# Optimization experiments

Measured on AMD Instinct MI355X. Metric: run time of the kernel, lower is better.

The kernel has to match this reference:

```python
import jax, jax.numpy as jnp
import numpy as np

B, S, I, H = 64, 1024, 256, 256  # batch, seq_len, input_size, hidden_size (2 layers)


def _gru_layer(x, W_ih, W_hh, b_ih, b_hh):
    """Run a torch.nn.GRUCell-equivalent layer over time. x: [B,S,in] -> [B,S,H]."""
    Hd = W_hh.shape[1]
    # Precompute input-side gate projections for all timesteps (math-equivalent).
    xg = jnp.einsum('bsi,gi->bsg', x, W_ih) + b_ih  # [B,S,3H]

    def step(h, xg_t):
        hg = h @ W_hh.T + b_hh                      # [B,3H]
        xr, xz, xn = jnp.split(xg_t, 3, axis=-1)
        hr, hz, hn = jnp.split(hg, 3, axis=-1)
        r = jax.nn.sigmoid(xr + hr)
        z = jax.nn.sigmoid(xz + hz)
        n = jnp.tanh(xn + r * hn)
        h_new = (1.0 - z) * n + z * h
        return h_new, h_new

    h0 = jnp.zeros((x.shape[0], Hd), dtype=x.dtype)
    _, hs = jax.lax.scan(step, h0, jnp.swapaxes(xg, 0, 1))  # scan over time
    return jnp.swapaxes(hs, 0, 1)  # [B,S,H]


def setup_inputs() -> dict:
    key = jax.random.key(0)
    ks = jax.random.split(key, 9)
    s_i = 1.0 / np.sqrt(H)
    u = lambda k, shape: jax.random.uniform(k, shape, jnp.float32, -s_i, s_i)
    return {
        'inputs': jax.random.normal(ks[0], (B, S, I), dtype=jnp.float32),
        'W_ih0': u(ks[1], (3 * H, I)),
        'W_hh0': u(ks[2], (3 * H, H)),
        'b_ih0': u(ks[3], (3 * H,)),
        'b_hh0': u(ks[4], (3 * H,)),
        'W_ih1': u(ks[5], (3 * H, H)),
        'W_hh1': u(ks[6], (3 * H, H)),
        'b_ih1': u(ks[7], (3 * H,)),
        'b_hh1': u(ks[8], (3 * H,)),
    }


def reference(inputs, W_ih0, W_hh0, b_ih0, b_hh0, W_ih1, W_hh1, b_ih1, b_hh1):
    h1 = _gru_layer(inputs, W_ih0, W_hh0, b_ih0, b_hh0)  # layer 0 states [B,S,H]
    h2 = _gru_layer(h1, W_ih1, W_hh1, b_ih1, b_hh1)      # layer 1 states [B,S,H]
    # return_sequences=True: (last-layer states, concat of all layers' states)
    return h2, jnp.concatenate([h1, h2], axis=2)
```

## Files before the change

kernel.cpp:

```cpp
#include <hip/hip_runtime.h>
#include <hip/hip_fp16.h>

#define BB 64
#define SS 1024
#define HD 256
#define GG 768

typedef _Float16 h2_t __attribute__((ext_vector_type(2)));
typedef _Float16 h8_t __attribute__((ext_vector_type(8)));

#define FDOT2(a, b, c) __builtin_amdgcn_fdot2((a), (b), (c), false)

__device__ __forceinline__ float sigm(float x) {
    return 1.0f / (1.0f + __expf(-x));
}
__device__ __forceinline__ float tanh_fast(float x) {
    float e = __expf(2.0f * fabsf(x));
    float t = 1.0f - 2.0f / (e + 1.0f);
    return copysignf(t, x);
}

__device__ __forceinline__ void load_wrow(const float* W, int g, h2_t* w) {
    const float2* wrow = (const float2*)(W + (size_t)g * 256);
#pragma unroll
    for (int k = 0; k < 128; k++) {
        float2 f = wrow[k];
        h2_t p; p.x = (_Float16)f.x; p.y = (_Float16)f.y;
        w[k] = p;
    }
}

__device__ __forceinline__ float dot256(const h8_t* hv, const h2_t* w, float acc) {
#pragma unroll
    for (int k = 0; k < 32; k++) {
        h8_t v = hv[k];
        h2_t p0, p1, p2, p3;
        p0.x = v[0]; p0.y = v[1];
        p1.x = v[2]; p1.y = v[3];
        p2.x = v[4]; p2.y = v[5];
        p3.x = v[6]; p3.y = v[7];
        acc = FDOT2(w[4 * k + 0], p0, acc);
        acc = FDOT2(w[4 * k + 1], p1, acc);
        acc = FDOT2(w[4 * k + 2], p2, acc);
        acc = FDOT2(w[4 * k + 3], p3, acc);
    }
    return acc;
}

__device__ __forceinline__ void wait_ge(unsigned* f, unsigned v) {
    if (threadIdx.x == 0) {
        while (__hip_atomic_load(f, __ATOMIC_RELAXED, __HIP_MEMORY_SCOPE_AGENT) < v)
            __builtin_amdgcn_s_sleep(2);
        (void)__hip_atomic_load(f, __ATOMIC_ACQUIRE, __HIP_MEMORY_SCOPE_AGENT);
    }
    __syncthreads();
}
__device__ __forceinline__ void publish(unsigned* f, unsigned v) {
    __syncthreads();
    if (threadIdx.x == 0)
        __hip_atomic_store(f, v, __ATOMIC_RELEASE, __HIP_MEMORY_SCOPE_AGENT);
}

__global__ __launch_bounds__(GG, 3) void gru_pipe(
    const float* __restrict__ X,
    const float* __restrict__ Wih0, const float* __restrict__ bih0,
    const float* __restrict__ Whh0, const float* __restrict__ bhh0,
    const float* __restrict__ Wih1, const float* __restrict__ bih1,
    const float* __restrict__ Whh1, const float* __restrict__ bhh1,
    float* __restrict__ h2out, float* __restrict__ cat,
    float* __restrict__ ring0, float* __restrict__ ring1,
    unsigned* __restrict__ prog, int CT, int NS, int NC)
{
    __shared__ h8_t xs[2048];
    __shared__ float hf[HD], rs[HD], zs[HD];

    const int role = blockIdx.x >> 6;
    const int b    = blockIdx.x & 63;
    const int g    = threadIdx.x;

    unsigned* f_p0 = prog + (0 * 64 + b) * 16;
    unsigned* f_p1 = prog + (1 * 64 + b) * 16;
    unsigned* f_r0 = prog + (2 * 64 + b) * 16;
    unsigned* f_r1 = prog + (3 * 64 + b) * 16;

    h2_t w[128];

    if (role == 0 || role == 1) {
        const float* Wp   = (role == 0) ? Wih0 : Wih1;
        const float* bp   = (role == 0) ? bih0 : bih1;
        const float* Xs   = (role == 0) ? X : cat;
        const int xstride = (role == 0) ? 256 : 512;
        float* ringo      = (role == 0) ? ring0 : ring1;
        unsigned* f_up    = (role == 0) ? nullptr : f_r0;
        unsigned* f_cons  = (role == 0) ? f_r0 : f_r1;
        unsigned* f_out   = (role == 0) ? f_p0 : f_p1;

        load_wrow(Wp, g, w);
        const float bg = bp[g];
        _Float16* xsh = (_Float16*)xs;

        for (int c = 0; c < NC; c++) {
            if (f_up) wait_ge(f_up, c + 1);
            if (c >= NS) wait_ge(f_cons, c - NS + 1);
            const int t0 = c * CT;
            for (int idx = g; idx < CT * 256; idx += GG) {
                int tt = idx >> 8, k = idx & 255;
                xsh[idx] = (_Float16)Xs[((size_t)b * SS + t0 + tt) * xstride + k];
            }
            __syncthreads();
            float* ro = ringo + ((size_t)b * NS + (c % NS)) * ((size_t)CT * GG) + g;
            for (int tt = 0; tt < CT; tt++) {
                float acc = dot256(&xs[tt * 32], w, bg);
                ro[(size_t)tt * GG] = acc;
            }
            publish(f_out, c + 1);
        }
    } else {
        const float* Wp    = (role == 2) ? Whh0 : Whh1;
        const float* bp    = (role == 2) ? bhh0 : bhh1;
        const float* ringi = (role == 2) ? ring0 : ring1;
        unsigned* f_in  = (role == 2) ? f_p0 : f_p1;
        unsigned* f_out = (role == 2) ? f_r0 : f_r1;
        float* outA   = (role == 2) ? cat : h2out;
        int   strideA = (role == 2) ? 512 : 256;
        float* outB   = (role == 2) ? nullptr : (cat + 256);

        load_wrow(Wp, g, w);
        const float bg = bp[g];
        const int cls = g >> 8;
        const int i   = g & 255;

        if (g < HD) { hf[g] = 0.0f; ((_Float16*)xs)[g] = (_Float16)0.0f; }
        __syncthreads();

        for (int c = 0; c < NC; c++) {
            wait_ge(f_in, c + 1);
            const float* xgp = ringi + ((size_t)b * NS + (c % NS)) * ((size_t)CT * GG) + g;
            float xv = xgp[0];
            for (int tt = 0; tt < CT; tt++) {
                float xv_next = (tt + 1 < CT) ? xgp[(size_t)(tt + 1) * GG] : 0.0f;
                float acc = dot256(xs, w, bg);
                if (cls == 0)      rs[i] = sigm(xv + acc);
                else if (cls == 1) zs[i] = sigm(xv + acc);
                __syncthreads();
                if (cls == 2) {
                    float r = rs[i], z = zs[i], hp = hf[i];
                    float n = tanh_fast(xv + r * acc);
                    float hnew = (1.0f - z) * n + z * hp;
                    hf[i] = hnew;
                    ((_Float16*)xs)[i] = (_Float16)hnew;
                    size_t t = (size_t)(c * CT + tt);
                    outA[((size_t)b * SS + t) * strideA + i] = hnew;
                    if (outB) outB[((size_t)b * SS + t) * 512 + i] = hnew;
                }
                __syncthreads();
                xv = xv_next;
            }
            publish(f_out, c + 1);
        }
    }
}

extern "C" void kernel_launch(void* const* d_in, const int* in_sizes, int n_in,
                              void* d_out, int out_size, void* d_ws, size_t ws_size,
                              hipStream_t stream)
{
    const float* inputs = (const float*)d_in[0];
    const float* W_ih0  = (const float*)d_in[1];
    const float* W_hh0  = (const float*)d_in[2];
    const float* b_ih0  = (const float*)d_in[3];
    const float* b_hh0  = (const float*)d_in[4];
    const float* W_ih1  = (const float*)d_in[5];
    const float* W_hh1  = (const float*)d_in[6];
    const float* b_ih1  = (const float*)d_in[7];
    const float* b_hh1  = (const float*)d_in[8];

    float* h2out = (float*)d_out;
    float* cat   = h2out + (size_t)BB * SS * HD;

    unsigned char* ws = (unsigned char*)d_ws;
    unsigned* prog = (unsigned*)ws;
    const size_t FLAG_BYTES = 4 * 64 * 16 * sizeof(unsigned);
    size_t avail = ws_size > FLAG_BYTES ? ws_size - FLAG_BYTES : 0;

    int CT = 64, NS = 0;
    for (;;) {
        size_t slot = (size_t)BB * CT * GG * sizeof(float);
        size_t m = slot ? avail / (2 * slot) : 0;
        int nc = SS / CT;
        NS = (int)(m < (size_t)nc ? m : (size_t)nc);
        if (NS >= 2 || CT == 8) break;
        CT >>= 1;
    }
    if (NS < 1) NS = 1;
    int NC = SS / CT;

    float* ring0 = (float*)(ws + FLAG_BYTES);
    float* ring1 = ring0 + (size_t)BB * NS * CT * GG;

    hipMemsetAsync(prog, 0, FLAG_BYTES, stream);
    gru_pipe<<<256, GG, 0, stream>>>(inputs,
                                     W_ih0, b_ih0, W_hh0, b_hh0,
                                     W_ih1, b_ih1, W_hh1, b_hh1,
                                     h2out, cat, ring0, ring1, prog, CT, NS, NC);
}
```

Measured before the change: 1.877 ms.

## Split gate dot products across lane quads with DPP reduction and swizzled LDS

Each thread now computes partial dot products for four gate rows over a 64-element slice of the hidden or input vector, instead of one full 256-length row. The four partials are combined with a DPP quad reduction. The shared-memory vector is stored with an XOR-style swizzle so that lanes reading different slices avoid bank conflicts. The old scheme had every lane read the same broadcast LDS addresses; the new one has each lane read only a quarter of the vector per row group, which cuts LDS traffic per FMA. The cost is extra cross-lane reduction ops and select logic on the serial recurrent critical path.

Result: faster. 1.812 ms (-3.5%).

```diff
diff --git a/kernel.cpp b/kernel.cpp
--- a/kernel.cpp
+++ b/kernel.cpp
@@ -20,31 +20,50 @@
     return copysignf(t, x);
 }
 
-__device__ __forceinline__ void load_wrow(const float* W, int g, h2_t* w) {
-    const float2* wrow = (const float2*)(W + (size_t)g * 256);
-#pragma unroll
-    for (int k = 0; k < 128; k++) {
-        float2 f = wrow[k];
-        h2_t p; p.x = (_Float16)f.x; p.y = (_Float16)f.y;
-        w[k] = p;
-    }
-}
-
-__device__ __forceinline__ float dot256(const h8_t* hv, const h2_t* w, float acc) {
-#pragma unroll
-    for (int k = 0; k < 32; k++) {
-        h8_t v = hv[k];
+__device__ __forceinline__ float quad_reduce(float x) {
+    int t = __builtin_amdgcn_update_dpp(0, __float_as_int(x), 0xB1, 0xF, 0xF, true);
+    x += __int_as_float(t);
+    t = __builtin_amdgcn_update_dpp(0, __float_as_int(x), 0x4E, 0xF, 0xF, true);
+    x += __int_as_float(t);
+    return x;
+}
+
+__device__ __forceinline__ void load_wslices(const float* W, int wv, int row, int sl, h2_t w[4][32]) {
+#pragma unroll
+    for (int q = 0; q < 4; q++) {
+        const float2* wr = (const float2*)(W + (size_t)(wv * 64 + row + 16 * q) * 256 + sl * 64);
+#pragma unroll
+        for (int k = 0; k < 32; k++) {
+            float2 f = wr[k];
+            h2_t p; p.x = (_Float16)f.x; p.y = (_Float16)f.y;
+            w[q][k] = p;
+        }
+    }
+}
+
+__device__ __forceinline__ int swz256(int k) {
+    int ksl = k >> 6;
+    return ksl * 128 + ((((k >> 3) & 7) + 2 * ksl) & 7) * 16 + (k & 7) * 2;
+}
+
+__device__ __forceinline__ void dot_slices(const char* tbase, int sl, const h2_t w[4][32], float acc[4]) {
+    const char* base = tbase + sl * 128;
+#pragma unroll
+    for (int j = 0; j < 8; j++) {
+        h8_t v = *(const h8_t*)(base + ((((j + 2 * sl) & 7)) << 4));
         h2_t p0, p1, p2, p3;
         p0.x = v[0]; p0.y = v[1];
         p1.x = v[2]; p1.y = v[3];
         p2.x = v[4]; p2.y = v[5];
         p3.x = v[6]; p3.y = v[7];
-        acc = FDOT2(w[4 * k + 0], p0, acc);
-        acc = FDOT2(w[4 * k + 1], p1, acc);
-        acc = FDOT2(w[4 * k + 2], p2, acc);
-        acc = FDOT2(w[4 * k + 3], p3, acc);
-    }
-    return acc;
+#pragma unroll
+        for (int q = 0; q < 4; q++) {
+            acc[q] = FDOT2(w[q][4 * j + 0], p0, acc[q]);
+            acc[q] = FDOT2(w[q][4 * j + 1], p1, acc[q]);
+            acc[q] = FDOT2(w[q][4 * j + 2], p2, acc[q]);
+            acc[q] = FDOT2(w[q][4 * j + 3], p3, acc[q]);
+        }
+    }
 }
 
 __device__ __forceinline__ void wait_ge(unsigned* f, unsigned v) {
@@ -77,13 +96,18 @@
     const int role = blockIdx.x >> 6;
     const int b    = blockIdx.x & 63;
     const int g    = threadIdx.x;
+    const int wv   = g >> 6;
+    const int l    = g & 63;
+    const int row  = l >> 2;
+    const int sl   = l & 3;
+    const int out  = wv * 64 + row + 16 * sl;
 
     unsigned* f_p0 = prog + (0 * 64 + b) * 16;
     unsigned* f_p1 = prog + (1 * 64 + b) * 16;
     unsigned* f_r0 = prog + (2 * 64 + b) * 16;
     unsigned* f_r1 = prog + (3 * 64 + b) * 16;
 
-    h2_t w[128];
+    h2_t w[4][32];
 
     if (role == 0 || role == 1) {
         const float* Wp   = (role == 0) ? Wih0 : Wih1;
@@ -95,9 +119,9 @@
         unsigned* f_cons  = (role == 0) ? f_r0 : f_r1;
         unsigned* f_out   = (role == 0) ? f_p0 : f_p1;
 
-        load_wrow(Wp, g, w);
-        const float bg = bp[g];
-        _Float16* xsh = (_Float16*)xs;
+        load_wslices(Wp, wv, row, sl, w);
+        const float bv = bp[out];
+        char* xb = (char*)xs;
 
         for (int c = 0; c < NC; c++) {
             if (f_up) wait_ge(f_up, c + 1);
@@ -105,13 +129,20 @@
             const int t0 = c * CT;
             for (int idx = g; idx < CT * 256; idx += GG) {
                 int tt = idx >> 8, k = idx & 255;
-                xsh[idx] = (_Float16)Xs[((size_t)b * SS + t0 + tt) * xstride + k];
+                *(_Float16*)(xb + tt * 512 + swz256(k)) =
+                    (_Float16)Xs[((size_t)b * SS + t0 + tt) * xstride + k];
             }
             __syncthreads();
-            float* ro = ringo + ((size_t)b * NS + (c % NS)) * ((size_t)CT * GG) + g;
+            float* ro = ringo + ((size_t)b * NS + (c % NS)) * ((size_t)CT * GG) + out;
             for (int tt = 0; tt < CT; tt++) {
-                float acc = dot256(&xs[tt * 32], w, bg);
-                ro[(size_t)tt * GG] = acc;
+                float acc[4] = {0.f, 0.f, 0.f, 0.f};
+                dot_slices(xb + tt * 512, sl, w, acc);
+                float g0 = quad_reduce(acc[0]);
+                float g1 = quad_reduce(acc[1]);
+                float g2 = quad_reduce(acc[2]);
+                float g3 = quad_reduce(acc[3]);
+                float mine = (sl == 0) ? g0 : (sl == 1) ? g1 : (sl == 2) ? g2 : g3;
+                ro[(size_t)tt * GG] = mine + bv;
             }
             publish(f_out, c + 1);
         }
@@ -125,30 +156,38 @@
         int   strideA = (role == 2) ? 512 : 256;
         float* outB   = (role == 2) ? nullptr : (cat + 256);
 
-        load_wrow(Wp, g, w);
-        const float bg = bp[g];
-        const int cls = g >> 8;
-        const int i   = g & 255;
-
-        if (g < HD) { hf[g] = 0.0f; ((_Float16*)xs)[g] = (_Float16)0.0f; }
+        load_wslices(Wp, wv, row, sl, w);
+        const float bv = bp[out];
+        const int cls = wv >> 2;
+        const int i   = out & 255;
+        char* xb = (char*)xs;
+        _Float16* hws = (_Float16*)(xb + swz256(i));
+
+        if (g < HD) { hf[g] = 0.0f; ((unsigned short*)xs)[g] = 0; }
         __syncthreads();
 
         for (int c = 0; c < NC; c++) {
             wait_ge(f_in, c + 1);
-            const float* xgp = ringi + ((size_t)b * NS + (c % NS)) * ((size_t)CT * GG) + g;
+            const float* xgp = ringi + ((size_t)b * NS + (c % NS)) * ((size_t)CT * GG) + out;
             float xv = xgp[0];
             for (int tt = 0; tt < CT; tt++) {
                 float xv_next = (tt + 1 < CT) ? xgp[(size_t)(tt + 1) * GG] : 0.0f;
-                float acc = dot256(xs, w, bg);
-                if (cls == 0)      rs[i] = sigm(xv + acc);
-                else if (cls == 1) zs[i] = sigm(xv + acc);
+                float acc[4] = {0.f, 0.f, 0.f, 0.f};
+                dot_slices(xb, sl, w, acc);
+                float g0 = quad_reduce(acc[0]);
+                float g1 = quad_reduce(acc[1]);
+                float g2 = quad_reduce(acc[2]);
+                float g3 = quad_reduce(acc[3]);
+                float hd = ((sl == 0) ? g0 : (sl == 1) ? g1 : (sl == 2) ? g2 : g3) + bv;
+                if (cls == 0)      rs[i] = sigm(xv + hd);
+                else if (cls == 1) zs[i] = sigm(xv + hd);
                 __syncthreads();
                 if (cls == 2) {
                     float r = rs[i], z = zs[i], hp = hf[i];
-                    float n = tanh_fast(xv + r * acc);
+                    float n = tanh_fast(xv + r * hd);
                     float hnew = (1.0f - z) * n + z * hp;
                     hf[i] = hnew;
-                    ((_Float16*)xs)[i] = (_Float16)hnew;
+                    *hws = (_Float16)hnew;
                     size_t t = (size_t)(c * CT + tt);
                     outA[((size_t)b * SS + t) * strideA + i] = hnew;
                     if (outB) outB[((size_t)b * SS + t) * 512 + i] = hnew;
```

## Batch 16 sequences per block and compute GRU gates with MFMA

Applied to the files above, without the earlier changes.

Replaces the per-sequence dot-product blocks (256 blocks of 768 threads using fdot2) with 16 blocks of 256 threads. Each block handles 16 batch rows and computes gate matmuls with 16x16x32 f16 MFMA, keeping weight fragments in registers. The recurrent hidden state stays in registers and goes through a swizzled, double-buffered LDS tile. The r/z hidden biases are folded into the input projection. The aim is to cut the serial per-step cost and the synchronisation count, at the price of far fewer active CUs, very high register pressure from 96 weight fragments per thread, and scattered output stores.

Measured after the change: 7.443 ms. 3.97x slower.

```diff
diff --git a/kernel.cpp b/kernel.cpp
--- a/kernel.cpp
+++ b/kernel.cpp
@@ -5,11 +5,12 @@
 #define SS 1024
 #define HD 256
 #define GG 768
-
-typedef _Float16 h2_t __attribute__((ext_vector_type(2)));
-typedef _Float16 h8_t __attribute__((ext_vector_type(8)));
-
-#define FDOT2(a, b, c) __builtin_amdgcn_fdot2((a), (b), (c), false)
+#define NT 256
+
+typedef _Float16 v8h __attribute__((ext_vector_type(8)));
+typedef float v4f __attribute__((ext_vector_type(4)));
+
+#define MFMA_F16(a, b, c) __builtin_amdgcn_mfma_f32_16x16x32_f16((a), (b), (c), 0, 0, 0)
 
 __device__ __forceinline__ float sigm(float x) {
     return 1.0f / (1.0f + __expf(-x));
@@ -20,31 +21,33 @@
     return copysignf(t, x);
 }
 
-__device__ __forceinline__ void load_wrow(const float* W, int g, h2_t* w) {
-    const float2* wrow = (const float2*)(W + (size_t)g * 256);
-#pragma unroll
-    for (int k = 0; k < 128; k++) {
-        float2 f = wrow[k];
-        h2_t p; p.x = (_Float16)f.x; p.y = (_Float16)f.y;
-        w[k] = p;
-    }
-}
-
-__device__ __forceinline__ float dot256(const h8_t* hv, const h2_t* w, float acc) {
-#pragma unroll
-    for (int k = 0; k < 32; k++) {
-        h8_t v = hv[k];
-        h2_t p0, p1, p2, p3;
-        p0.x = v[0]; p0.y = v[1];
-        p1.x = v[2]; p1.y = v[3];
-        p2.x = v[4]; p2.y = v[5];
-        p3.x = v[6]; p3.y = v[7];
-        acc = FDOT2(w[4 * k + 0], p0, acc);
-        acc = FDOT2(w[4 * k + 1], p1, acc);
-        acc = FDOT2(w[4 * k + 2], p2, acc);
-        acc = FDOT2(w[4 * k + 3], p3, acc);
-    }
-    return acc;
+__device__ __forceinline__ v8h load_bfrag(const float* W, int tile, int kk, int l) {
+    int n  = ((tile >> 4) << 8) + ((tile & 15) << 4) + (l & 15);
+    int k0 = (kk << 5) + ((l >> 4) << 3);
+    const float4* p = (const float4*)(W + (size_t)n * 256 + k0);
+    float4 f0 = p[0], f1 = p[1];
+    v8h r;
+    r[0] = (_Float16)f0.x; r[1] = (_Float16)f0.y; r[2] = (_Float16)f0.z; r[3] = (_Float16)f0.w;
+    r[4] = (_Float16)f1.x; r[5] = (_Float16)f1.y; r[6] = (_Float16)f1.z; r[7] = (_Float16)f1.w;
+    return r;
+}
+
+__device__ __forceinline__ v8h read_afrag(const char* base, int kk, int l) {
+    int row = l & 15;
+    int off = row * 512 + (kk << 6) + ((l >> 4) << 4);
+    off ^= (row & 7) << 4;
+    return *(const v8h*)(base + off);
+}
+
+__device__ __forceinline__ void cvt_store16(char* dst, int sbase, int swz,
+                                            float4 f0, float4 f1, float4 f2, float4 f3) {
+    v8h a, b;
+    a[0] = (_Float16)f0.x; a[1] = (_Float16)f0.y; a[2] = (_Float16)f0.z; a[3] = (_Float16)f0.w;
+    a[4] = (_Float16)f1.x; a[5] = (_Float16)f1.y; a[6] = (_Float16)f1.z; a[7] = (_Float16)f1.w;
+    b[0] = (_Float16)f2.x; b[1] = (_Float16)f2.y; b[2] = (_Float16)f2.z; b[3] = (_Float16)f2.w;
+    b[4] = (_Float16)f3.x; b[5] = (_Float16)f3.y; b[6] = (_Float16)f3.z; b[7] = (_Float16)f3.w;
+    *(v8h*)(dst + ((sbase + 0) ^ swz)) = a;
+    *(v8h*)(dst + ((sbase + 16) ^ swz)) = b;
 }
 
 __device__ __forceinline__ void wait_ge(unsigned* f, unsigned v) {
@@ -61,7 +64,7 @@
         __hip_atomic_store(f, v, __ATOMIC_RELEASE, __HIP_MEMORY_SCOPE_AGENT);
 }
 
-__global__ __launch_bounds__(GG, 3) void gru_pipe(
+__global__ __launch_bounds__(NT, 1) void gru_pipe(
     const float* __restrict__ X,
     const float* __restrict__ Wih0, const float* __restrict__ bih0,
     const float* __restrict__ Whh0, const float* __restrict__ bhh0,
@@ -71,23 +74,27 @@
     float* __restrict__ ring0, float* __restrict__ ring1,
     unsigned* __restrict__ prog, int CT, int NS, int NC)
 {
-    __shared__ h8_t xs[2048];
-    __shared__ float hf[HD], rs[HD], zs[HD];
-
-    const int role = blockIdx.x >> 6;
-    const int b    = blockIdx.x & 63;
+    __shared__ __align__(16) char lds[16384];
+
+    const int role = blockIdx.x >> 2;
+    const int bg   = blockIdx.x & 3;
     const int g    = threadIdx.x;
-
-    unsigned* f_p0 = prog + (0 * 64 + b) * 16;
-    unsigned* f_p1 = prog + (1 * 64 + b) * 16;
-    unsigned* f_r0 = prog + (2 * 64 + b) * 16;
-    unsigned* f_r1 = prog + (3 * 64 + b) * 16;
-
-    h2_t w[128];
-
-    if (role == 0 || role == 1) {
+    const int wv   = g >> 6;
+    const int l    = g & 63;
+    const int lo   = l & 15;
+    const int grp  = l >> 4;
+
+    unsigned* f_p0 = prog + (0 * 4 + bg) * 16;
+    unsigned* f_p1 = prog + (1 * 4 + bg) * 16;
+    unsigned* f_r0 = prog + (2 * 4 + bg) * 16;
+    unsigned* f_r1 = prog + (3 * 4 + bg) * 16;
+
+    v8h wB[12][8];
+
+    if (role <= 1) {
         const float* Wp   = (role == 0) ? Wih0 : Wih1;
-        const float* bp   = (role == 0) ? bih0 : bih1;
+        const float* bi   = (role == 0) ? bih0 : bih1;
+        const float* bh   = (role == 0) ? bhh0 : bhh1;
         const float* Xs   = (role == 0) ? X : cat;
         const int xstride = (role == 0) ? 256 : 512;
         float* ringo      = (role == 0) ? ring0 : ring1;
@@ -95,29 +102,72 @@
         unsigned* f_cons  = (role == 0) ? f_r0 : f_r1;
         unsigned* f_out   = (role == 0) ? f_p0 : f_p1;
 
-        load_wrow(Wp, g, w);
-        const float bg = bp[g];
-        _Float16* xsh = (_Float16*)xs;
+        float bias[12];
+#pragma unroll
+        for (int t12 = 0; t12 < 12; t12++) {
+            int tile = wv * 12 + t12;
+            int n = ((tile >> 4) << 8) + ((tile & 15) << 4) + lo;
+            bias[t12] = bi[n] + (tile < 32 ? bh[n] : 0.0f);
+#pragma unroll
+            for (int kk = 0; kk < 8; kk++) wB[t12][kk] = load_bfrag(Wp, tile, kk, l);
+        }
+
+        const int srow  = g >> 4;
+        const int scol  = (g & 15) << 4;
+        const int swz   = (srow & 7) << 4;
+        const int sbase = srow * 512 + ((g & 15) << 5);
+        const size_t srowbase = (size_t)(bg * 16 + srow) * SS;
 
         for (int c = 0; c < NC; c++) {
             if (f_up) wait_ge(f_up, c + 1);
             if (c >= NS) wait_ge(f_cons, c - NS + 1);
-            const int t0 = c * CT;
-            for (int idx = g; idx < CT * 256; idx += GG) {
-                int tt = idx >> 8, k = idx & 255;
-                xsh[idx] = (_Float16)Xs[((size_t)b * SS + t0 + tt) * xstride + k];
+            {
+                const float* src = Xs + (srowbase + (size_t)c * CT) * xstride + scol;
+                cvt_store16(lds, sbase, swz,
+                            ((const float4*)src)[0], ((const float4*)src)[1],
+                            ((const float4*)src)[2], ((const float4*)src)[3]);
             }
             __syncthreads();
-            float* ro = ringo + ((size_t)b * NS + (c % NS)) * ((size_t)CT * GG) + g;
+            float* ringc = ringo + ((size_t)(bg * NS + (c % NS)) * CT) * 12288;
             for (int tt = 0; tt < CT; tt++) {
-                float acc = dot256(&xs[tt * 32], w, bg);
-                ro[(size_t)tt * GG] = acc;
+                float4 f0, f1, f2, f3;
+                const bool pre = (tt + 1 < CT);
+                if (pre) {
+                    const float* src = Xs + (srowbase + (size_t)(c * CT + tt + 1)) * xstride + scol;
+                    f0 = ((const float4*)src)[0]; f1 = ((const float4*)src)[1];
+                    f2 = ((const float4*)src)[2]; f3 = ((const float4*)src)[3];
+                }
+                const char* abuf = lds + ((tt & 1) << 13);
+                v4f acc[12];
+#pragma unroll
+                for (int t12 = 0; t12 < 12; t12++) {
+                    float bv = bias[t12];
+                    acc[t12] = (v4f){bv, bv, bv, bv};
+                }
+                v8h Aa = read_afrag(abuf, 0, l), Ab = read_afrag(abuf, 1, l);
+#pragma unroll
+                for (int kk = 0; kk < 8; kk++) {
+                    v8h Ac = (kk & 1) ? Ab : Aa;
+#pragma unroll
+                    for (int t12 = 0; t12 < 12; t12++)
+                        acc[t12] = MFMA_F16(Ac, wB[t12][kk], acc[t12]);
+                    if (kk + 2 < 8) {
+                        if (kk & 1) Ab = read_afrag(abuf, kk + 2, l);
+                        else        Aa = read_afrag(abuf, kk + 2, l);
+                    }
+                }
+                if (pre)
+                    cvt_store16(lds + (((tt + 1) & 1) << 13), sbase, swz, f0, f1, f2, f3);
+                v4f* rp = (v4f*)(ringc + (size_t)tt * 12288);
+#pragma unroll
+                for (int t12 = 0; t12 < 12; t12++) rp[(wv * 12 + t12) * 64 + l] = acc[t12];
+                __syncthreads();
             }
             publish(f_out, c + 1);
         }
     } else {
         const float* Wp    = (role == 2) ? Whh0 : Whh1;
-        const float* bp    = (role == 2) ? bhh0 : bhh1;
+        const float* bh    = (role == 2) ? bhh0 : bhh1;
         const float* ringi = (role == 2) ? ring0 : ring1;
         unsigned* f_in  = (role == 2) ? f_p0 : f_p1;
         unsigned* f_out = (role == 2) ? f_r0 : f_r1;
@@ -125,36 +175,97 @@
         int   strideA = (role == 2) ? 512 : 256;
         float* outB   = (role == 2) ? nullptr : (cat + 256);
 
-        load_wrow(Wp, g, w);
-        const float bg = bp[g];
-        const int cls = g >> 8;
-        const int i   = g & 255;
-
-        if (g < HD) { hf[g] = 0.0f; ((_Float16*)xs)[g] = (_Float16)0.0f; }
+#pragma unroll
+        for (int t12 = 0; t12 < 12; t12++) {
+            int tile = ((t12 >> 2) << 4) + wv * 4 + (t12 & 3);
+#pragma unroll
+            for (int kk = 0; kk < 8; kk++) wB[t12][kk] = load_bfrag(Wp, tile, kk, l);
+        }
+        float bn[4];
+#pragma unroll
+        for (int sub = 0; sub < 4; sub++) bn[sub] = bh[512 + wv * 64 + sub * 16 + lo];
+
+        ((float4*)lds)[g]       = (float4){0.f, 0.f, 0.f, 0.f};
+        ((float4*)lds)[g + 256] = (float4){0.f, 0.f, 0.f, 0.f};
         __syncthreads();
+
+        float hp[4][4];
+#pragma unroll
+        for (int s = 0; s < 4; s++)
+#pragma unroll
+            for (int q = 0; q < 4; q++) hp[s][q] = 0.0f;
+
+        v4f aR[4], aZ[4], aN[4], xnv[4];
 
         for (int c = 0; c < NC; c++) {
             wait_ge(f_in, c + 1);
-            const float* xgp = ringi + ((size_t)b * NS + (c % NS)) * ((size_t)CT * GG) + g;
-            float xv = xgp[0];
+            const float* ringc = ringi + ((size_t)(bg * NS + (c % NS)) * CT) * 12288;
+            {
+                const v4f* rp = (const v4f*)ringc;
+#pragma unroll
+                for (int sub = 0; sub < 4; sub++) {
+                    aR[sub]  = rp[(wv * 4 + sub) * 64 + l];
+                    aZ[sub]  = rp[(16 + wv * 4 + sub) * 64 + l];
+                    xnv[sub] = rp[(32 + wv * 4 + sub) * 64 + l];
+                    float bv = bn[sub];
+                    aN[sub] = (v4f){bv, bv, bv, bv};
+                }
+            }
             for (int tt = 0; tt < CT; tt++) {
-                float xv_next = (tt + 1 < CT) ? xgp[(size_t)(tt + 1) * GG] : 0.0f;
-                float acc = dot256(xs, w, bg);
-                if (cls == 0)      rs[i] = sigm(xv + acc);
-                else if (cls == 1) zs[i] = sigm(xv + acc);
+                const int t = c * CT + tt;
+                const char* hbuf = lds + ((t & 1) << 13);
+                char* hbufn      = lds + (((t + 1) & 1) << 13);
+
+                v8h Aa = read_afrag(hbuf, 0, l), Ab = read_afrag(hbuf, 1, l);
+#pragma unroll
+                for (int kk = 0; kk < 8; kk++) {
+                    v8h Ac = (kk & 1) ? Ab : Aa;
+#pragma unroll
+                    for (int s = 0; s < 4; s++) aR[s] = MFMA_F16(Ac, wB[s][kk], aR[s]);
+#pragma unroll
+                    for (int s = 0; s < 4; s++) aZ[s] = MFMA_F16(Ac, wB[4 + s][kk], aZ[s]);
+#pragma unroll
+                    for (int s = 0; s < 4; s++) aN[s] = MFMA_F16(Ac, wB[8 + s][kk], aN[s]);
+                    if (kk + 2 < 8) {
+                        if (kk & 1) Ab = read_afrag(hbuf, kk + 2, l);
+                        else        Aa = read_afrag(hbuf, kk + 2, l);
+                    }
+                }
+#pragma unroll
+                for (int sub = 0; sub < 4; sub++)
+#pragma unroll
+                    for (int q = 0; q < 4; q++) {
+                        float r = sigm(aR[sub][q]);
+                        float z = sigm(aZ[sub][q]);
+                        float n = tanh_fast(xnv[sub][q] + r * aN[sub][q]);
+                        hp[sub][q] = (1.0f - z) * n + z * hp[sub][q];
+                    }
+                if (tt + 1 < CT) {
+                    const v4f* rp = (const v4f*)(ringc + (size_t)(tt + 1) * 12288);
+#pragma unroll
+                    for (int sub = 0; sub < 4; sub++) {
+                        aR[sub]  = rp[(wv * 4 + sub) * 64 + l];
+                        aZ[sub]  = rp[(16 + wv * 4 + sub) * 64 + l];
+                        xnv[sub] = rp[(32 + wv * 4 + sub) * 64 + l];
+                        float bv = bn[sub];
+                        aN[sub] = (v4f){bv, bv, bv, bv};
+                    }
+                }
+#pragma unroll
+                for (int sub = 0; sub < 4; sub++) {
+                    int col = wv * 64 + sub * 16 + lo;
+#pragma unroll
+                    for (int q = 0; q < 4; q++) {
+                        int row = grp * 4 + q;
+                        float h = hp[sub][q];
+                        *(_Float16*)(hbufn + ((row * 512 + col * 2) ^ ((row & 7) << 4))) =
+                            (_Float16)h;
+                        size_t gb = (size_t)(bg * 16 + row) * SS + t;
+                        outA[gb * strideA + col] = h;
+                        if (outB) outB[gb * 512 + col] = h;
+                    }
+                }
                 __syncthreads();
-                if (cls == 2) {
-                    float r = rs[i], z = zs[i], hp = hf[i];
-                    float n = tanh_fast(xv + r * acc);
-                    float hnew = (1.0f - z) * n + z * hp;
-                    hf[i] = hnew;
-                    ((_Float16*)xs)[i] = (_Float16)hnew;
-                    size_t t = (size_t)(c * CT + tt);
-                    outA[((size_t)b * SS + t) * strideA + i] = hnew;
-                    if (outB) outB[((size_t)b * SS + t) * 512 + i] = hnew;
-                }
-                __syncthreads();
-                xv = xv_next;
             }
             publish(f_out, c + 1);
         }
@@ -199,8 +310,8 @@
     float* ring1 = ring0 + (size_t)BB * NS * CT * GG;
 
     hipMemsetAsync(prog, 0, FLAG_BYTES, stream);
-    gru_pipe<<<256, GG, 0, stream>>>(inputs,
-                                     W_ih0, b_ih0, W_hh0, b_hh0,
-                                     W_ih1, b_ih1, W_hh1, b_hh1,
-                                     h2out, cat, ring0, ring1, prog, CT, NS, NC);
-}
+    gru_pipe<<<16, NT, 0, stream>>>(inputs,
+                                    W_ih0, b_ih0, W_hh0, b_hh0,
+                                    W_ih1, b_ih1, W_hh1, b_hh1,
+                                    h2out, cat, ring0, ring1, prog, CT, NS, NC);
+}
```

## Remap GRU threads to pairs per hidden unit computing all three gates

Applied to the files above, without the earlier changes.

Each hidden unit is now handled by a pair of lanes. Each lane holds half of the r, z and n weight rows and computes all three gate dot products, and a DPP swap combines the two halves. This removes the per-step rs/zs LDS exchange and one of the two block barriers in the recurrent loop. The hidden state is double-buffered in LDS so only a single barrier per timestep is needed, blocks shrink from 768 to 512 threads, and input staging uses float4 loads. The cost is more registers per thread for three weight half-rows and duplicated gate math across the lane pair.

Measured after the change: 1.695 ms. 1.11x faster.

```diff
diff --git a/kernel.cpp b/kernel.cpp
--- a/kernel.cpp
+++ b/kernel.cpp
@@ -5,8 +5,10 @@
 #define SS 1024
 #define HD 256
 #define GG 768
+#define NT 512
 
 typedef _Float16 h2_t __attribute__((ext_vector_type(2)));
+typedef _Float16 h4_t __attribute__((ext_vector_type(4)));
 typedef _Float16 h8_t __attribute__((ext_vector_type(8)));
 
 #define FDOT2(a, b, c) __builtin_amdgcn_fdot2((a), (b), (c), false)
@@ -20,31 +22,42 @@
     return copysignf(t, x);
 }
 
-__device__ __forceinline__ void load_wrow(const float* W, int g, h2_t* w) {
-    const float2* wrow = (const float2*)(W + (size_t)g * 256);
+__device__ __forceinline__ float pair_reduce(float x) {
+    int t = __builtin_amdgcn_update_dpp(0, __float_as_int(x), 0xB1, 0xF, 0xF, true);
+    return x + __int_as_float(t);
+}
+
+__device__ __forceinline__ void load_wrow_half(const float* W, int row, int sl, h2_t wreg[64]) {
+    const float2* p = (const float2*)(W + (size_t)row * 256 + sl * 128);
 #pragma unroll
-    for (int k = 0; k < 128; k++) {
-        float2 f = wrow[k];
-        h2_t p; p.x = (_Float16)f.x; p.y = (_Float16)f.y;
-        w[k] = p;
-    }
-}
-
-__device__ __forceinline__ float dot256(const h8_t* hv, const h2_t* w, float acc) {
+    for (int k = 0; k < 64; k++) {
+        float2 f = p[k];
+        h2_t q; q.x = (_Float16)f.x; q.y = (_Float16)f.y;
+        wreg[k] = q;
+    }
+}
+
+__device__ __forceinline__ void dot3(const char* base, const h2_t w0[64], const h2_t w1[64],
+                                     const h2_t w2[64], float& a0, float& a1, float& a2) {
 #pragma unroll
-    for (int k = 0; k < 32; k++) {
-        h8_t v = hv[k];
+    for (int j = 0; j < 16; j++) {
+        h8_t v = *(const h8_t*)(base + j * 16);
         h2_t p0, p1, p2, p3;
         p0.x = v[0]; p0.y = v[1];
         p1.x = v[2]; p1.y = v[3];
         p2.x = v[4]; p2.y = v[5];
         p3.x = v[6]; p3.y = v[7];
-        acc = FDOT2(w[4 * k + 0], p0, acc);
-        acc = FDOT2(w[4 * k + 1], p1, acc);
-        acc = FDOT2(w[4 * k + 2], p2, acc);
-        acc = FDOT2(w[4 * k + 3], p3, acc);
-    }
-    return acc;
+        a0 = FDOT2(w0[4 * j + 0], p0, a0); a0 = FDOT2(w0[4 * j + 1], p1, a0);
+        a0 = FDOT2(w0[4 * j + 2], p2, a0); a0 = FDOT2(w0[4 * j + 3], p3, a0);
+        a1 = FDOT2(w1[4 * j + 0], p0, a1); a1 = FDOT2(w1[4 * j + 1], p1, a1);
+        a1 = FDOT2(w1[4 * j + 2], p2, a1); a1 = FDOT2(w1[4 * j + 3], p3, a1);
+        a2 = FDOT2(w2[4 * j + 0], p0, a2); a2 = FDOT2(w2[4 * j + 1], p1, a2);
+        a2 = FDOT2(w2[4 * j + 2], p2, a2); a2 = FDOT2(w2[4 * j + 3], p3, a2);
+    }
+}
+
+__device__ __forceinline__ void barrier_lds() {
+    asm volatile("s_waitcnt lgkmcnt(0)\n\ts_barrier" ::: "memory");
 }
 
 __device__ __forceinline__ void wait_ge(unsigned* f, unsigned v) {
@@ -61,7 +74,7 @@
         __hip_atomic_store(f, v, __ATOMIC_RELEASE, __HIP_MEMORY_SCOPE_AGENT);
 }
 
-__global__ __launch_bounds__(GG, 3) void gru_pipe(
+__global__ __launch_bounds__(NT, 2) void gru_pipe(
     const float* __restrict__ X,
     const float* __restrict__ Wih0, const float* __restrict__ bih0,
     const float* __restrict__ Whh0, const float* __restrict__ bhh0,
@@ -71,21 +84,24 @@
     float* __restrict__ ring0, float* __restrict__ ring1,
     unsigned* __restrict__ prog, int CT, int NS, int NC)
 {
-    __shared__ h8_t xs[2048];
-    __shared__ float hf[HD], rs[HD], zs[HD];
+    __shared__ __align__(16) char lds[32768];
 
     const int role = blockIdx.x >> 6;
     const int b    = blockIdx.x & 63;
     const int g    = threadIdx.x;
+    const int wv   = g >> 6;
+    const int l    = g & 63;
+    const int i    = wv * 32 + (l >> 1);
+    const int sl   = l & 1;
 
     unsigned* f_p0 = prog + (0 * 64 + b) * 16;
     unsigned* f_p1 = prog + (1 * 64 + b) * 16;
     unsigned* f_r0 = prog + (2 * 64 + b) * 16;
     unsigned* f_r1 = prog + (3 * 64 + b) * 16;
 
-    h2_t w[128];
-
-    if (role == 0 || role == 1) {
+    h2_t w0[64], w1[64], w2[64];
+
+    if (role <= 1) {
         const float* Wp   = (role == 0) ? Wih0 : Wih1;
         const float* bp   = (role == 0) ? bih0 : bih1;
         const float* Xs   = (role == 0) ? X : cat;
@@ -95,23 +111,36 @@
         unsigned* f_cons  = (role == 0) ? f_r0 : f_r1;
         unsigned* f_out   = (role == 0) ? f_p0 : f_p1;
 
-        load_wrow(Wp, g, w);
-        const float bg = bp[g];
-        _Float16* xsh = (_Float16*)xs;
+        load_wrow_half(Wp, i, sl, w0);
+        load_wrow_half(Wp, 256 + i, sl, w1);
+        load_wrow_half(Wp, 512 + i, sl, w2);
+        const float b0 = bp[i], b1 = bp[256 + i], b2 = bp[512 + i];
+        char* xb = (char*)lds;
 
         for (int c = 0; c < NC; c++) {
             if (f_up) wait_ge(f_up, c + 1);
             if (c >= NS) wait_ge(f_cons, c - NS + 1);
             const int t0 = c * CT;
-            for (int idx = g; idx < CT * 256; idx += GG) {
-                int tt = idx >> 8, k = idx & 255;
-                xsh[idx] = (_Float16)Xs[((size_t)b * SS + t0 + tt) * xstride + k];
+            for (int idx4 = g; idx4 < CT * 64; idx4 += NT) {
+                int tt = idx4 >> 6, k4 = idx4 & 63;
+                const float4* src = (const float4*)(Xs + ((size_t)b * SS + t0 + tt) * xstride);
+                float4 f = src[k4];
+                h4_t q;
+                q[0] = (_Float16)f.x; q[1] = (_Float16)f.y;
+                q[2] = (_Float16)f.z; q[3] = (_Float16)f.w;
+                *(h4_t*)(xb + tt * 512 + k4 * 8) = q;
             }
             __syncthreads();
-            float* ro = ringo + ((size_t)b * NS + (c % NS)) * ((size_t)CT * GG) + g;
+            float* ringc = ringo + ((size_t)b * NS + (c % NS)) * ((size_t)CT * GG);
             for (int tt = 0; tt < CT; tt++) {
-                float acc = dot256(&xs[tt * 32], w, bg);
-                ro[(size_t)tt * GG] = acc;
+                float a0 = 0.f, a1 = 0.f, a2 = 0.f;
+                dot3(xb + tt * 512 + sl * 256, w0, w1, w2, a0, a1, a2);
+                float pr = pair_reduce(a0) + b0;
+                float pz = pair_reduce(a1) + b1;
+                float pn = pair_reduce(a2) + b2;
+                float* rt = ringc + (size_t)tt * GG;
+                if (sl == 0) { rt[i] = pr; rt[256 + i] = pz; }
+                else         { rt[512 + i] = pn; }
             }
             publish(f_out, c + 1);
         }
@@ -121,40 +150,45 @@
         const float* ringi = (role == 2) ? ring0 : ring1;
         unsigned* f_in  = (role == 2) ? f_p0 : f_p1;
         unsigned* f_out = (role == 2) ? f_r0 : f_r1;
-        float* outA   = (role == 2) ? cat : h2out;
-        int   strideA = (role == 2) ? 512 : 256;
-        float* outB   = (role == 2) ? nullptr : (cat + 256);
-
-        load_wrow(Wp, g, w);
-        const float bg = bp[g];
-        const int cls = g >> 8;
-        const int i   = g & 255;
-
-        if (g < HD) { hf[g] = 0.0f; ((_Float16*)xs)[g] = (_Float16)0.0f; }
+
+        load_wrow_half(Wp, i, sl, w0);
+        load_wrow_half(Wp, 256 + i, sl, w1);
+        load_wrow_half(Wp, 512 + i, sl, w2);
+        const float b0 = bp[i], b1 = bp[256 + i], b2 = bp[512 + i];
+        char* xb = (char*)lds;
+
+        if (g < 128) ((float*)xb)[g] = 0.0f;
         __syncthreads();
+        float hp = 0.0f;
 
         for (int c = 0; c < NC; c++) {
             wait_ge(f_in, c + 1);
-            const float* xgp = ringi + ((size_t)b * NS + (c % NS)) * ((size_t)CT * GG) + g;
-            float xv = xgp[0];
+            const float* ringc = ringi + ((size_t)b * NS + (c % NS)) * ((size_t)CT * GG);
             for (int tt = 0; tt < CT; tt++) {
-                float xv_next = (tt + 1 < CT) ? xgp[(size_t)(tt + 1) * GG] : 0.0f;
-                float acc = dot256(xs, w, bg);
-                if (cls == 0)      rs[i] = sigm(xv + acc);
-                else if (cls == 1) zs[i] = sigm(xv + acc);
-                __syncthreads();
-                if (cls == 2) {
-                    float r = rs[i], z = zs[i], hp = hf[i];
-                    float n = tanh_fast(xv + r * acc);
-                    float hnew = (1.0f - z) * n + z * hp;
-                    hf[i] = hnew;
-                    ((_Float16*)xs)[i] = (_Float16)hnew;
-                    size_t t = (size_t)(c * CT + tt);
-                    outA[((size_t)b * SS + t) * strideA + i] = hnew;
-                    if (outB) outB[((size_t)b * SS + t) * 512 + i] = hnew;
+                const int t = c * CT + tt;
+                const char* hb = xb + ((t & 1) << 9);
+                char* hbn      = xb + (((t + 1) & 1) << 9);
+                const float* xgp = ringc + (size_t)tt * GG;
+                float xr = xgp[i], xz = xgp[256 + i], xn = xgp[512 + i];
+                float a0 = 0.f, a1 = 0.f, a2 = 0.f;
+                dot3(hb + sl * 256, w0, w1, w2, a0, a1, a2);
+                float hr = pair_reduce(a0) + b0;
+                float hz = pair_reduce(a1) + b1;
+                float hn = pair_reduce(a2) + b2;
+                float rg = sigm(xr + hr);
+                float zg = sigm(xz + hz);
+                float ng = tanh_fast(xn + rg * hn);
+                float hnew = (1.0f - zg) * ng + zg * hp;
+                hp = hnew;
+                if (sl == 0) *(_Float16*)(hbn + i * 2) = (_Float16)hnew;
+                size_t tb = (size_t)b * SS + t;
+                if (role == 2) {
+                    if (sl) cat[tb * 512 + i] = hnew;
+                } else {
+                    if (sl) h2out[tb * 256 + i] = hnew;
+                    else    cat[tb * 512 + 256 + i] = hnew;
                 }
-                __syncthreads();
-                xv = xv_next;
+                barrier_lds();
             }
             publish(f_out, c + 1);
         }
@@ -199,7 +233,7 @@
     float* ring1 = ring0 + (size_t)BB * NS * CT * GG;
 
     hipMemsetAsync(prog, 0, FLAG_BYTES, stream);
-    gru_pipe<<<256, GG, 0, stream>>>(inputs,
+    gru_pipe<<<256, NT, 0, stream>>>(inputs,
                                      W_ih0, b_ih0, W_hh0, b_hh0,
                                      W_ih1, b_ih1, W_hh1, b_hh1,
                                      h2out, cat, ring0, ring1, prog, CT, NS, NC);
```
